# Performance work log

Measured on AMD Instinct MI355X. Metric: run time of the kernel, lower is better.

Reference implementation:

```python
import jax, jax.numpy as jnp
import numpy as np


def gcn_conv(x, W, b, src, dst, num_nodes):
    # PyG GCNConv: h = D^{-1/2} (A + I) D^{-1/2} (x W) + b
    h = x @ W  # [N, H]
    ones = jnp.ones(src.shape[0], dtype=h.dtype)
    deg = jax.ops.segment_sum(ones, dst, num_segments=num_nodes) + 1.0  # +1 for self-loop
    d_inv_sqrt = jax.lax.rsqrt(deg)
    norm = d_inv_sqrt[src] * d_inv_sqrt[dst]  # [E]
    msg = h[src] * norm[:, None]  # [E, H] gather
    agg = jax.ops.segment_sum(msg, dst, num_segments=num_nodes)  # scatter-add
    agg = agg + h * (1.0 / deg)[:, None]  # self-loop term: deg_i^{-1/2} * deg_i^{-1/2}
    return agg + b


def setup_inputs() -> dict:
    key = jax.random.key(0)
    ks = jax.random.split(key, 10)
    N, E, F, H, C, G = 100000, 1000000, 64, 128, 2, 512
    x = jax.random.normal(ks[0], (N, F), dtype=jnp.float32)
    edge_index = jax.random.randint(ks[1], (2, E), 0, N, dtype=jnp.int64)
    batch = jnp.sort(jax.random.randint(ks[2], (N,), 0, G, dtype=jnp.int64))
    s1 = 1.0 / np.sqrt(F)
    s2 = 1.0 / np.sqrt(H)
    W1 = jax.random.normal(ks[3], (F, H), dtype=jnp.float32) * s1
    b1 = jnp.zeros((H,), dtype=jnp.float32)
    W2 = jax.random.normal(ks[4], (H, H), dtype=jnp.float32) * s2
    b2 = jnp.zeros((H,), dtype=jnp.float32)
    Wfc = jax.random.normal(ks[5], (H, C), dtype=jnp.float32) * s2
    bfc = jnp.zeros((C,), dtype=jnp.float32)
    return {"x": x, "edge_index": edge_index, "batch": batch, "num_graphs": G,
            "W1": W1, "b1": b1, "W2": W2, "b2": b2, "Wfc": Wfc, "bfc": bfc}


def reference(x, edge_index, batch, num_graphs, W1, b1, W2, b2, Wfc, bfc):
    # Dropout is inference-mode (identity), matching model.eval().
    N = x.shape[0]
    src, dst = edge_index[0], edge_index[1]
    h = gcn_conv(x, W1, b1, src, dst, N)
    h = jax.nn.relu(h)
    h = gcn_conv(h, W2, b2, src, dst, N)
    h = jax.nn.relu(h)
    # global mean pool over graphs
    summed = jax.ops.segment_sum(h, batch, num_segments=num_graphs)  # [G, H]
    counts = jax.ops.segment_sum(jnp.ones((N,), h.dtype), batch, num_segments=num_graphs)
    pooled = summed / jnp.maximum(counts, 1.0)[:, None]
    logits = pooled @ Wfc + bfc  # [G, C]
    return jax.nn.softmax(logits, axis=1)
```

## Files before the change

### kernel.cpp

```cpp
#include <hip/hip_runtime.h>
#include <hip/hip_bf16.h>

typedef __hip_bfloat16 bf16;
typedef __attribute__((ext_vector_type(8))) short short8;
typedef __attribute__((ext_vector_type(4))) float f32x4;
typedef __attribute__((ext_vector_type(2))) float f32x2;

#define FDIM 64
#define HDIM 128

#define ESTRIDE 4096
#define EC 8192
#define ECPT (EC / 256)

__device__ __forceinline__ float b2f(bf16 v) { return __bfloat162float(v); }
__device__ __forceinline__ float bits2f(unsigned int u) {
    return __uint_as_float(u << 16);
}
__device__ __forceinline__ unsigned short f2bits(float f) {
    bf16 b = __float2bfloat16(f);
    return *reinterpret_cast<unsigned short*>(&b);
}
__device__ __forceinline__ unsigned char f2fp8(float v) {
    int pk = __builtin_amdgcn_cvt_pk_fp8_f32(v, v, 0, false);
    return (unsigned char)(pk & 0xFF);
}

__device__ __forceinline__ int edge_word(const int* e, long long logical_idx, int is64) {
    return is64 ? e[2 * logical_idx] : e[logical_idx];
}

__global__ __launch_bounds__(256) void k_phase1(const int* __restrict__ edge,
                                                int* __restrict__ gcur,
                                                int* __restrict__ ebuf,
                                                int E,
                                                const void* __restrict__ W1, const void* __restrict__ b1,
                                                const void* __restrict__ W2, const void* __restrict__ b2,
                                                const void* __restrict__ Wfc, const void* __restrict__ bfc,
                                                bf16* __restrict__ W1t, bf16* __restrict__ W2t,
                                                bf16* __restrict__ b1c, bf16* __restrict__ b2c,
                                                bf16* __restrict__ Wfcc, bf16* __restrict__ bfcc,
                                                const void* __restrict__ x,
                                                unsigned char* __restrict__ X8,
                                                int totalX4,
                                                int* __restrict__ flags,
                                                const int* __restrict__ batch,
                                                int* __restrict__ gstart,
                                                int N, int G,
                                                int NB1, int WB, int XB) {
    int blk = blockIdx.x;
    int tid = threadIdx.x;
    if (blk < NB1) {
        unsigned long long zb = __ballot(edge[2 * (tid & 63) + 1] == 0);
        int is64 = (__popcll(zb) > 32);
        __shared__ int h[512];
        for (int b2 = tid; b2 < 512; b2 += 256) h[b2] = 0;
        __syncthreads();
        int e0 = blk * EC;
        int dcache[ECPT];
#pragma unroll
        for (int k = 0; k < ECPT; k++) {
            int i = e0 + (k << 8) + tid;
            int d = -1;
            if (i < E) d = edge_word(edge, (long long)E + i, is64);
            dcache[k] = d;
            if (d >= 0) atomicAdd(&h[(d >> 8) & 511], 1);
        }
        __syncthreads();
        for (int b2 = tid; b2 < 512; b2 += 256) {
            int c = h[b2];
            h[b2] = c ? atomicAdd(&gcur[b2], c) : 0;
        }
        __syncthreads();
#pragma unroll
        for (int k = 0; k < ECPT; k++) {
            int i = e0 + (k << 8) + tid;
            int d = dcache[k];
            if (d >= 0) {
                int s = edge_word(edge, i, is64);
                int bb = (d >> 8) & 511;
                int pos = atomicAdd(&h[bb], 1);
                if ((unsigned)pos < (unsigned)ESTRIDE)
                    ebuf[(bb << 12) + pos] = s | ((d & 255) << 24);
            }
        }
    } else if (blk < NB1 + WB) {
        const unsigned short* w1u = (const unsigned short*)W1;
        unsigned short wv = w1u[2 * (tid & 63)];
        int ee = (wv >> 7) & 0xFF;
        unsigned long long wb2 = __ballot(ee == 0 || ee >= 137);
        int f0 = (__popcll(wb2) > 4);
        if (blk == NB1 && tid == 0) flags[0] = f0;
        int gid = (blk - NB1) * 256 + tid;
        int stride = WB * 256;
#define CV(src, si) (f0 ? __float2bfloat16(((const float*)(src))[si]) : ((const bf16*)(src))[si])
        for (int i = gid; i < FDIM * HDIM; i += stride) {
            int n = i >> 6, k = i & 63;
            W1t[i] = CV(W1, k * HDIM + n);
        }
        for (int i = gid; i < HDIM * HDIM; i += stride) {
            int n = i >> 7, k = i & 127;
            W2t[i] = CV(W2, k * HDIM + n);
        }
        for (int i = gid; i < HDIM; i += stride) b1c[i] = CV(b1, i);
        for (int i = gid; i < HDIM; i += stride) b2c[i] = CV(b2, i);
        for (int i = gid; i < HDIM * 2; i += stride) Wfcc[i] = CV(Wfc, i);
        for (int i = gid; i < 2; i += stride) bfcc[i] = CV(bfc, i);
#undef CV
    } else if (blk < NB1 + WB + XB) {
        const unsigned short* w1u = (const unsigned short*)W1;
        unsigned short wv = w1u[2 * (tid & 63)];
        int ee = (wv >> 7) & 0xFF;
        unsigned long long wb2 = __ballot(ee == 0 || ee >= 137);
        int f0 = (__popcll(wb2) > 4);
        int t = (blk - NB1 - WB) * 256 + tid;
        if (t >= totalX4) return;
        float4 v;
        if (f0) {
            v = ((const float4*)x)[t];
        } else {
            uint2 p = ((const uint2*)x)[t];
            v.x = bits2f(p.x & 0xFFFFu); v.y = bits2f(p.x >> 16);
            v.z = bits2f(p.y & 0xFFFFu); v.w = bits2f(p.y >> 16);
        }
        unsigned int q0 = (unsigned int)__builtin_amdgcn_cvt_pk_fp8_f32(v.x, v.y, 0, false) & 0xFFFFu;
        unsigned int q1 = (unsigned int)__builtin_amdgcn_cvt_pk_fp8_f32(v.z, v.w, 0, false) & 0xFFFFu;
        ((unsigned int*)X8)[t] = (q1 << 16) | q0;
    } else {
        int bv = batch[1025 + 2 * (tid & 63)];
        unsigned long long bb2 = __ballot(bv == 0);
        int is64 = (__popcll(bb2) > 32);
        int i = (blk - NB1 - WB - XB) * 256 + tid;
        if (i >= N) return;
        int bi = is64 ? batch[2 * i] : batch[i];
        if (i == 0) {
            for (int g = 0; g <= bi; g++) gstart[g] = 0;
        } else {
            int bp = is64 ? batch[2 * (i - 1)] : batch[i - 1];
            for (int g = bp + 1; g <= bi; g++) gstart[g] = i;
        }
        if (i == N - 1) {
            for (int g = bi + 1; g <= G; g++) gstart[g] = N;
        }
    }
}

__global__ __launch_bounds__(256) void k_csr(const int* __restrict__ ebuf,
                                             const int* __restrict__ gcur,
                                             int* __restrict__ rowptr,
                                             int* __restrict__ cnt,
                                             float* __restrict__ dinv,
                                             int* __restrict__ srclist,
                                             int* __restrict__ perm,
                                             int N) {
    __shared__ int sred[256];
    __shared__ int sc[256];
    __shared__ int sa[256], sb[256];
    __shared__ int dh[33];
    int b = blockIdx.x;
    int tid = threadIdx.x;
    int part = 0;
    for (int j = tid; j < b; j += 256) {
        int v = gcur[j];
        part += (v > ESTRIDE) ? ESTRIDE : v;
    }
    sred[tid] = part;
    __syncthreads();
    for (int s = 128; s > 0; s >>= 1) {
        if (tid < s) sred[tid] += sred[tid + s];
        __syncthreads();
    }
    int gbase = sred[0];
    int cnt_b = gcur[b];
    if (cnt_b > ESTRIDE) cnt_b = ESTRIDE;
    sc[tid] = 0;
    __syncthreads();
    const int* eb = ebuf + (b << 12);
    for (int j = tid; j < cnt_b; j += 256) {
        int p = eb[j];
        atomicAdd(&sc[(unsigned)p >> 24], 1);
    }
    __syncthreads();
    int cval = sc[tid];
    sa[tid] = cval;
    __syncthreads();
    int* cur = sa; int* nxt = sb;
    for (int off = 1; off < 256; off <<= 1) {
        int v = cur[tid];
        if (tid >= off) v += cur[tid - off];
        nxt[tid] = v;
        __syncthreads();
        int* t = cur; cur = nxt; nxt = t;
    }
    int excl = cur[tid] - cval;
    int node = (b << 8) + tid;
    if (node < N) {
        rowptr[node] = gbase + excl;
        cnt[node] = cval;
        dinv[node] = rsqrtf((float)cval + 1.0f);
    }
    __syncthreads();
    sc[tid] = excl;
    __syncthreads();
    for (int j = tid; j < cnt_b; j += 256) {
        int p = eb[j];
        int pos = atomicAdd(&sc[(unsigned)p >> 24], 1);
        srclist[gbase + pos] = p & 0xFFFFFF;
    }
    if (tid < 33) dh[tid] = 0;
    perm[(b << 8) + tid] = N;
    __syncthreads();
    int bin = -1;
    if (node < N) {
        int c = (cval < 32) ? cval : 32;
        bin = 32 - c;
        atomicAdd(&dh[bin], 1);
    }
    __syncthreads();
    if (tid == 0) {
        int acc2 = 0;
        for (int k = 0; k < 33; k++) { int t = dh[k]; dh[k] = acc2; acc2 += t; }
    }
    __syncthreads();
    if (bin >= 0) {
        int pos = atomicAdd(&dh[bin], 1);
        perm[(b << 8) + pos] = node;
    }
}

#define ACCFP8(u2, e) do { \
    f32x2 f01 = __builtin_amdgcn_cvt_pk_f32_fp8((u2).x, false); \
    f32x2 f23 = __builtin_amdgcn_cvt_pk_f32_fp8((u2).x, true); \
    f32x2 f45 = __builtin_amdgcn_cvt_pk_f32_fp8((u2).y, false); \
    f32x2 f67 = __builtin_amdgcn_cvt_pk_f32_fp8((u2).y, true); \
    acc[0] += f01[0] * (e); acc[1] += f01[1] * (e); \
    acc[2] += f23[0] * (e); acc[3] += f23[1] * (e); \
    acc[4] += f45[0] * (e); acc[5] += f45[1] * (e); \
    acc[6] += f67[0] * (e); acc[7] += f67[1] * (e); } while (0)

__global__ __launch_bounds__(256) void k_agg64(const unsigned char* __restrict__ x8,
                                               const int* __restrict__ srclist,
                                               const int* __restrict__ rowptr,
                                               const int* __restrict__ count,
                                               const float* __restrict__ dinv,
                                               const int* __restrict__ perm,
                                               bf16* __restrict__ outb, int N, int NR) {
    int wave = threadIdx.x >> 6;
    int lane = threadIdx.x & 63;
    int group = lane >> 3;
    int sub = lane & 7;
    int r = blockIdx.x * 32 + wave * 8 + group;
    int i = (r < NR) ? perm[r] : N;
    if (i >= N) return;
    int start = rowptr[i];
    int cnt = count[i];
    float di = dinv[i];
    const uint2* hrow = (const uint2*)x8;
    float acc[8] = {0.f, 0.f, 0.f, 0.f, 0.f, 0.f, 0.f, 0.f};
    int lb = group << 3;
    for (int jb = 0; jb < cnt; jb += 8) {
        int m = cnt - jb; if (m > 8) m = 8;
        int sv = srclist[start + jb + ((sub < m) ? sub : (m - 1))];
        float dvv = dinv[sv];
        if (m == 8) {
            int s[8]; float e[8]; uint2 v[8];
#pragma unroll
            for (int t = 0; t < 8; t++) { s[t] = __shfl(sv, lb + t); e[t] = __shfl(dvv, lb + t); }
#pragma unroll
            for (int t = 0; t < 8; t++) v[t] = hrow[(size_t)s[t] * 8 + sub];
#pragma unroll
            for (int t = 0; t < 8; t++) ACCFP8(v[t], e[t]);
        } else {
            int j = 0;
            for (; j + 4 <= m; j += 4) {
                int s0 = __shfl(sv, lb + j + 0); float e0 = __shfl(dvv, lb + j + 0);
                int s1 = __shfl(sv, lb + j + 1); float e1 = __shfl(dvv, lb + j + 1);
                int s2 = __shfl(sv, lb + j + 2); float e2 = __shfl(dvv, lb + j + 2);
                int s3 = __shfl(sv, lb + j + 3); float e3 = __shfl(dvv, lb + j + 3);
                uint2 v0 = hrow[(size_t)s0 * 8 + sub];
                uint2 v1 = hrow[(size_t)s1 * 8 + sub];
                uint2 v2 = hrow[(size_t)s2 * 8 + sub];
                uint2 v3 = hrow[(size_t)s3 * 8 + sub];
                ACCFP8(v0, e0); ACCFP8(v1, e1); ACCFP8(v2, e2); ACCFP8(v3, e3);
            }
            for (; j < m; j++) {
                int s0 = __shfl(sv, lb + j); float e0 = __shfl(dvv, lb + j);
                uint2 v0 = hrow[(size_t)s0 * 8 + sub];
                ACCFP8(v0, e0);
            }
        }
    }
    {
        uint2 vs = hrow[(size_t)i * 8 + sub];
        float self = di * di;
        float sacc[8] = {0.f};
        {
            float* acc = sacc;
            ACCFP8(vs, self);
        }
#pragma unroll
        for (int k = 0; k < 8; k++) acc[k] = di * acc[k] + sacc[k];
    }
    uint4 pv;
    pv.x = ((unsigned int)f2bits(acc[1]) << 16) | f2bits(acc[0]);
    pv.y = ((unsigned int)f2bits(acc[3]) << 16) | f2bits(acc[2]);
    pv.z = ((unsigned int)f2bits(acc[5]) << 16) | f2bits(acc[4]);
    pv.w = ((unsigned int)f2bits(acc[7]) << 16) | f2bits(acc[6]);
    ((uint4*)outb)[(size_t)i * 8 + sub] = pv;
}

__global__ __launch_bounds__(256) void k_agg128(const unsigned char* __restrict__ h8,
                                                const int* __restrict__ srclist,
                                                const int* __restrict__ rowptr,
                                                const int* __restrict__ count,
                                                const float* __restrict__ dinv,
                                                const int* __restrict__ perm,
                                                bf16* __restrict__ outb, int N, int NR) {
    int wave = threadIdx.x >> 6;
    int lane = threadIdx.x & 63;
    int group = lane >> 4;
    int sub = lane & 15;
    int r = blockIdx.x * 16 + wave * 4 + group;
    int i = (r < NR) ? perm[r] : N;
    if (i >= N) return;
    int start = rowptr[i];
    int cnt = count[i];
    float di = dinv[i];
    const uint2* hrow = (const uint2*)h8;
    float acc[8] = {0.f, 0.f, 0.f, 0.f, 0.f, 0.f, 0.f, 0.f};
    int lb = group << 4;
    for (int jb = 0; jb < cnt; jb += 16) {
        int m = cnt - jb; if (m > 16) m = 16;
        int sv = srclist[start + jb + ((sub < m) ? sub : (m - 1))];
        float dvv = dinv[sv];
        int j = 0;
        for (; j + 8 <= m; j += 8) {
            int s[8]; float e[8]; uint2 v[8];
#pragma unroll
            for (int t = 0; t < 8; t++) { s[t] = __shfl(sv, lb + j + t); e[t] = __shfl(dvv, lb + j + t); }
#pragma unroll
            for (int t = 0; t < 8; t++) v[t] = hrow[(size_t)s[t] * 16 + sub];
#pragma unroll
            for (int t = 0; t < 8; t++) ACCFP8(v[t], e[t]);
        }
        for (; j + 4 <= m; j += 4) {
            int s0 = __shfl(sv, lb + j + 0); float e0 = __shfl(dvv, lb + j + 0);
            int s1 = __shfl(sv, lb + j + 1); float e1 = __shfl(dvv, lb + j + 1);
            int s2 = __shfl(sv, lb + j + 2); float e2 = __shfl(dvv, lb + j + 2);
            int s3 = __shfl(sv, lb + j + 3); float e3 = __shfl(dvv, lb + j + 3);
            uint2 v0 = hrow[(size_t)s0 * 16 + sub];
            uint2 v1 = hrow[(size_t)s1 * 16 + sub];
            uint2 v2 = hrow[(size_t)s2 * 16 + sub];
            uint2 v3 = hrow[(size_t)s3 * 16 + sub];
            ACCFP8(v0, e0); ACCFP8(v1, e1); ACCFP8(v2, e2); ACCFP8(v3, e3);
        }
        for (; j < m; j++) {
            int s0 = __shfl(sv, lb + j); float e0 = __shfl(dvv, lb + j);
            uint2 v0 = hrow[(size_t)s0 * 16 + sub];
            ACCFP8(v0, e0);
        }
    }
    {
        uint2 vs = hrow[(size_t)i * 16 + sub];
        float self = di * di;
        float sacc[8] = {0.f};
        {
            float* acc = sacc;
            ACCFP8(vs, self);
        }
#pragma unroll
        for (int k = 0; k < 8; k++) acc[k] = di * acc[k] + sacc[k];
    }
    uint4 pv;
    pv.x = ((unsigned int)f2bits(acc[1]) << 16) | f2bits(acc[0]);
    pv.y = ((unsigned int)f2bits(acc[3]) << 16) | f2bits(acc[2]);
    pv.z = ((unsigned int)f2bits(acc[5]) << 16) | f2bits(acc[4]);
    pv.w = ((unsigned int)f2bits(acc[7]) << 16) | f2bits(acc[6]);
    ((uint4*)outb)[(size_t)i * 16 + sub] = pv;
}

#define K1PAD 72
__global__ __launch_bounds__(256) void k_gemmA(const bf16* __restrict__ Y,
                                               const bf16* __restrict__ W1t,
                                               const bf16* __restrict__ bias,
                                               unsigned char* __restrict__ h8, int N) {
    __shared__ bf16 As[64 * K1PAD];
    __shared__ bf16 Wt[HDIM * K1PAD];
    __shared__ float bsf[HDIM];
    int tid = threadIdx.x;
    int base = blockIdx.x * 64;
    {
        const uint4* wsrc = (const uint4*)W1t;
        for (int i = tid; i < HDIM * 8; i += 256) {
            int n = i >> 3, c = i & 7;
            *(uint4*)&Wt[n * K1PAD + c * 8] = wsrc[n * 8 + c];
        }
    }
    {
        const uint4* xb = (const uint4*)Y;
        for (int i = tid; i < 64 * 8; i += 256) {
            int r = i >> 3, c = i & 7;
            int gr = base + r; if (gr >= N) gr = N - 1;
            *(uint4*)&As[r * K1PAD + c * 8] = xb[(size_t)gr * 8 + c];
        }
    }
    if (tid < HDIM) bsf[tid] = b2f(bias[tid]);
    __syncthreads();
    int wid = tid >> 6, lane = tid & 63;
    int l15 = lane & 15, q = lane >> 4;
    int m0 = wid * 16;
    short8 af[2];
#pragma unroll
    for (int kc = 0; kc < 2; kc++)
        af[kc] = *(const short8*)&As[(m0 + l15) * K1PAD + kc * 32 + q * 8];
    f32x4 acc[8];
#pragma unroll
    for (int nt = 0; nt < 8; nt++) {
        acc[nt] = (f32x4){0.f, 0.f, 0.f, 0.f};
#pragma unroll
        for (int kc = 0; kc < 2; kc++) {
            short8 bf = *(const short8*)&Wt[(nt * 16 + l15) * K1PAD + kc * 32 + q * 8];
            acc[nt] = __builtin_amdgcn_mfma_f32_16x16x32_bf16(af[kc], bf, acc[nt], 0, 0, 0);
        }
    }
#pragma unroll
    for (int nt = 0; nt < 8; nt++) {
        int col = nt * 16 + l15;
        float bv = bsf[col];
#pragma unroll
        for (int r = 0; r < 4; r++) {
            int gr = base + m0 + q * 4 + r;
            if (gr < N) {
                float v = fmaxf(acc[nt][r] + bv, 0.f);
                h8[(size_t)gr * HDIM + col] = f2fp8(v);
            }
        }
    }
}

#define K2PAD 136
__global__ __launch_bounds__(256) void k_gemmB(const bf16* __restrict__ Z,
                                               const bf16* __restrict__ W2t,
                                               const bf16* __restrict__ bias,
                                               bf16* __restrict__ outp, int N) {
    __shared__ bf16 As[64 * K2PAD];
    __shared__ bf16 Wt[HDIM * K2PAD];
    __shared__ float bsf[HDIM];
    int tid = threadIdx.x;
    int base = blockIdx.x * 64;
    {
        const uint4* wsrc = (const uint4*)W2t;
        for (int i = tid; i < HDIM * 16; i += 256) {
            int n = i >> 4, c = i & 15;
            *(uint4*)&Wt[n * K2PAD + c * 8] = wsrc[n * 16 + c];
        }
    }
    const uint4* xb = (const uint4*)Z;
    for (int i = tid; i < 64 * 16; i += 256) {
        int r = i >> 4, c = i & 15;
        int gr = base + r; if (gr >= N) gr = N - 1;
        *(uint4*)&As[r * K2PAD + c * 8] = xb[(size_t)gr * 16 + c];
    }
    if (tid < HDIM) bsf[tid] = b2f(bias[tid]);
    __syncthreads();
    int wid = tid >> 6, lane = tid & 63;
    int l15 = lane & 15, q = lane >> 4;
    int m0 = wid * 16;
    short8 af[4];
#pragma unroll
    for (int kc = 0; kc < 4; kc++)
        af[kc] = *(const short8*)&As[(m0 + l15) * K2PAD + kc * 32 + q * 8];
    f32x4 acc[8];
#pragma unroll
    for (int nt = 0; nt < 8; nt++) {
        acc[nt] = (f32x4){0.f, 0.f, 0.f, 0.f};
#pragma unroll
        for (int kc = 0; kc < 4; kc++) {
            short8 bf = *(const short8*)&Wt[(nt * 16 + l15) * K2PAD + kc * 32 + q * 8];
            acc[nt] = __builtin_amdgcn_mfma_f32_16x16x32_bf16(af[kc], bf, acc[nt], 0, 0, 0);
        }
    }
#pragma unroll
    for (int nt = 0; nt < 8; nt++) {
        int col = nt * 16 + l15;
        float bv = bsf[col];
#pragma unroll
        for (int r = 0; r < 4; r++) {
            int gr = base + m0 + q * 4 + r;
            if (gr < N) outp[(size_t)gr * HDIM + col] = __float2bfloat16(fmaxf(acc[nt][r] + bv, 0.f));
        }
    }
}

__global__ __launch_bounds__(256) void k_pool(const bf16* __restrict__ hact,
                                              const int* __restrict__ gstart,
                                              const bf16* __restrict__ Wfc,
                                              const bf16* __restrict__ bfc,
                                              void* __restrict__ out,
                                              const int* __restrict__ flags) {
    __shared__ float lds[16][HDIM + 1];
    __shared__ float colsum[HDIM];
    int g = blockIdx.x;
    int s = gstart[g], e = gstart[g + 1];
    int tid = threadIdx.x;
    int cslot = tid & 15;
    int rslot = tid >> 4;
    const uint4* hp = (const uint4*)hact;
    float a[8] = {0.f, 0.f, 0.f, 0.f, 0.f, 0.f, 0.f, 0.f};
    for (int r = s + rslot; r < e; r += 16) {
        uint4 v = hp[(size_t)r * 16 + cslot];
        a[0] += bits2f(v.x & 0xFFFFu); a[1] += bits2f(v.x >> 16);
        a[2] += bits2f(v.y & 0xFFFFu); a[3] += bits2f(v.y >> 16);
        a[4] += bits2f(v.z & 0xFFFFu); a[5] += bits2f(v.z >> 16);
        a[6] += bits2f(v.w & 0xFFFFu); a[7] += bits2f(v.w >> 16);
    }
#pragma unroll
    for (int k = 0; k < 8; k++) lds[rslot][cslot * 8 + k] = a[k];
    __syncthreads();
    if (tid < HDIM) {
        float sum = 0.f;
#pragma unroll
        for (int k = 0; k < 16; k++) sum += lds[k][tid];
        colsum[tid] = sum;
    }
    __syncthreads();
    if (tid >= 64) return;
    int lane = tid;
    float inv = 1.0f / fmaxf((float)(e - s), 1.0f);
    float m0 = colsum[2 * lane] * inv;
    float m1 = colsum[2 * lane + 1] * inv;
    float l0 = m0 * b2f(Wfc[(2 * lane) * 2 + 0]) + m1 * b2f(Wfc[(2 * lane + 1) * 2 + 0]);
    float l1 = m0 * b2f(Wfc[(2 * lane) * 2 + 1]) + m1 * b2f(Wfc[(2 * lane + 1) * 2 + 1]);
    for (int sft = 32; sft; sft >>= 1) { l0 += __shfl_down(l0, sft); l1 += __shfl_down(l1, sft); }
    if (lane == 0) {
        float z0 = l0 + b2f(bfc[0]);
        float z1 = l1 + b2f(bfc[1]);
        float mx = fmaxf(z0, z1);
        float e0 = expf(z0 - mx), e1 = expf(z1 - mx);
        float sm = e0 + e1;
        float p0 = e0 / sm, p1 = e1 / sm;
        if (flags[0]) {
            ((float*)out)[2 * g + 0] = p0;
            ((float*)out)[2 * g + 1] = p1;
        } else {
            ((bf16*)out)[2 * g + 0] = __float2bfloat16(p0);
            ((bf16*)out)[2 * g + 1] = __float2bfloat16(p1);
        }
    }
}

extern "C" void kernel_launch(void* const* d_in, const int* in_sizes, int n_in,
                              void* d_out, int out_size, void* d_ws, size_t ws_size,
                              hipStream_t stream) {
    const void* x    = d_in[0];
    const int*  edge = (const int*)d_in[1];
    const int*  batch= (const int*)d_in[2];
    const void* W1  = d_in[4];
    const void* b1  = d_in[5];
    const void* W2  = d_in[6];
    const void* b2  = d_in[7];
    const void* Wfc = d_in[8];
    const void* bfc = d_in[9];

    int N = in_sizes[0] / FDIM;
    int E = in_sizes[1] / 2;
    int G = out_size / 2;

    int*   flags  = (int*)d_ws;
    float* dinv   = (float*)((char*)d_ws + 64);
    int*   gcur   = (int*)(dinv + N);
    int*   gstart = gcur + 512;
    int*   rowptr = gstart + 516;
    int*   count  = rowptr + N;
    int*   perm_  = count + N;
    int*   srclist= perm_ + 131072;
    int*   ebuf   = srclist + E;
    bf16*  Abuf   = (bf16*)(ebuf + 512 * ESTRIDE);
    bf16*  Bbuf   = Abuf + (size_t)N * HDIM;
    bf16*  b1c    = Bbuf + (size_t)N * HDIM;
    bf16*  b2c    = b1c + HDIM;
    bf16*  Wfcc   = b2c + HDIM;
    bf16*  bfcc   = Wfcc + 256;
    bf16*  W1t    = bfcc + 64;
    bf16*  W2t    = W1t + FDIM * HDIM;
    unsigned char* H8 = (unsigned char*)(W2t + HDIM * HDIM);
    unsigned char* X8 = H8 + (size_t)N * HDIM;

    bf16* Y = Abuf;
    bf16* Z = Abuf;

    int NB  = (N + 255) >> 8;
    int NR  = NB << 8;
    int NB1 = (E + EC - 1) / EC;
    int WB = 32;
    int XB = (N * 16 + 255) / 256;
    int BB = (N + 255) / 256;
    int totalX4 = N * 16;

    hipMemsetAsync(gcur, 0, 512 * sizeof(int), stream);
    k_phase1<<<NB1 + WB + XB + BB, 256, 0, stream>>>(edge, gcur, ebuf, E,
                                                     W1, b1, W2, b2, Wfc, bfc,
                                                     W1t, W2t, b1c, b2c, Wfcc, bfcc,
                                                     x, X8, totalX4, flags,
                                                     batch, gstart, N, G,
                                                     NB1, WB, XB);
    k_csr<<<NB, 256, 0, stream>>>(ebuf, gcur, rowptr, count, dinv, srclist, perm_, N);

    k_agg64<<<(NR + 31) / 32, 256, 0, stream>>>(X8, srclist, rowptr, count, dinv, perm_, Y, N, NR);
    k_gemmA<<<(N + 63) / 64, 256, 0, stream>>>(Y, W1t, b1c, H8, N);

    k_agg128<<<(NR + 15) / 16, 256, 0, stream>>>(H8, srclist, rowptr, count, dinv, perm_, Z, N, NR);
    k_gemmB<<<(N + 63) / 64, 256, 0, stream>>>(Z, W2t, b2c, Bbuf, N);

    k_pool<<<G, 256, 0, stream>>>(Bbuf, gstart, Wfcc, bfcc, d_out, flags);
}
```

Measured before the change: 245.6 us.

## Drop degree-sorted node permutation and widen aggregation lanes to 16-byte loads

Removes the per-block degree-binned permutation built in the CSR kernel, so both aggregation kernels process nodes in natural order. Each lane now loads 16 fp8 features (uint4) per neighbor instead of 8, halving lanes per node: 4 lanes per node for the 64-wide layer and 8 for the 128-wide layer. This cuts permutation overhead and the extra indirection, and widens memory transactions. In exchange, nodes with different degrees now share a wave, which can cause more divergence, and each lane holds more accumulator registers.

```diff
diff --git a/kernel.cpp b/kernel.cpp
--- a/kernel.cpp
+++ b/kernel.cpp
@@ -151,12 +151,10 @@
                                              int* __restrict__ cnt,
                                              float* __restrict__ dinv,
                                              int* __restrict__ srclist,
-                                             int* __restrict__ perm,
                                              int N) {
     __shared__ int sred[256];
     __shared__ int sc[256];
     __shared__ int sa[256], sb[256];
-    __shared__ int dh[33];
     int b = blockIdx.x;
     int tid = threadIdx.x;
     int part = 0;
@@ -207,69 +205,116 @@
         int pos = atomicAdd(&sc[(unsigned)p >> 24], 1);
         srclist[gbase + pos] = p & 0xFFFFFF;
     }
-    if (tid < 33) dh[tid] = 0;
-    perm[(b << 8) + tid] = N;
-    __syncthreads();
-    int bin = -1;
-    if (node < N) {
-        int c = (cval < 32) ? cval : 32;
-        bin = 32 - c;
-        atomicAdd(&dh[bin], 1);
-    }
-    __syncthreads();
-    if (tid == 0) {
-        int acc2 = 0;
-        for (int k = 0; k < 33; k++) { int t = dh[k]; dh[k] = acc2; acc2 += t; }
-    }
-    __syncthreads();
-    if (bin >= 0) {
-        int pos = atomicAdd(&dh[bin], 1);
-        perm[(b << 8) + pos] = node;
-    }
-}
-
-#define ACCFP8(u2, e) do { \
-    f32x2 f01 = __builtin_amdgcn_cvt_pk_f32_fp8((u2).x, false); \
-    f32x2 f23 = __builtin_amdgcn_cvt_pk_f32_fp8((u2).x, true); \
-    f32x2 f45 = __builtin_amdgcn_cvt_pk_f32_fp8((u2).y, false); \
-    f32x2 f67 = __builtin_amdgcn_cvt_pk_f32_fp8((u2).y, true); \
-    acc[0] += f01[0] * (e); acc[1] += f01[1] * (e); \
-    acc[2] += f23[0] * (e); acc[3] += f23[1] * (e); \
-    acc[4] += f45[0] * (e); acc[5] += f45[1] * (e); \
-    acc[6] += f67[0] * (e); acc[7] += f67[1] * (e); } while (0)
+}
+
+#define ACC4(w, e, o) do { \
+    f32x2 fA = __builtin_amdgcn_cvt_pk_f32_fp8((w), false); \
+    f32x2 fB = __builtin_amdgcn_cvt_pk_f32_fp8((w), true); \
+    acc[(o)+0] += fA[0] * (e); acc[(o)+1] += fA[1] * (e); \
+    acc[(o)+2] += fB[0] * (e); acc[(o)+3] += fB[1] * (e); } while (0)
+#define ACC16(u4, e) do { ACC4((u4).x, (e), 0); ACC4((u4).y, (e), 4); \
+                          ACC4((u4).z, (e), 8); ACC4((u4).w, (e), 12); } while (0)
+
+__device__ __forceinline__ uint4 packbf16x8(const float* a) {
+    uint4 p;
+    p.x = ((unsigned int)f2bits(a[1]) << 16) | f2bits(a[0]);
+    p.y = ((unsigned int)f2bits(a[3]) << 16) | f2bits(a[2]);
+    p.z = ((unsigned int)f2bits(a[5]) << 16) | f2bits(a[4]);
+    p.w = ((unsigned int)f2bits(a[7]) << 16) | f2bits(a[6]);
+    return p;
+}
 
 __global__ __launch_bounds__(256) void k_agg64(const unsigned char* __restrict__ x8,
                                                const int* __restrict__ srclist,
                                                const int* __restrict__ rowptr,
                                                const int* __restrict__ count,
                                                const float* __restrict__ dinv,
-                                               const int* __restrict__ perm,
-                                               bf16* __restrict__ outb, int N, int NR) {
+                                               bf16* __restrict__ outb, int N) {
+    int wave = threadIdx.x >> 6;
+    int lane = threadIdx.x & 63;
+    int group = lane >> 2;
+    int sub = lane & 3;
+    int i = blockIdx.x * 64 + wave * 16 + group;
+    if (i >= N) return;
+    int start = rowptr[i];
+    int cnt = count[i];
+    float di = dinv[i];
+    const uint4* hrow = (const uint4*)x8;
+    float acc[16];
+#pragma unroll
+    for (int k = 0; k < 16; k++) acc[k] = 0.f;
+    int lb = group << 2;
+    for (int jb = 0; jb < cnt; jb += 4) {
+        int m = cnt - jb; if (m > 4) m = 4;
+        int sv = srclist[start + jb + ((sub < m) ? sub : (m - 1))];
+        float dvv = dinv[sv];
+        if (m == 4) {
+            int s[4]; float e[4]; uint4 v[4];
+#pragma unroll
+            for (int t = 0; t < 4; t++) { s[t] = __shfl(sv, lb + t); e[t] = __shfl(dvv, lb + t); }
+#pragma unroll
+            for (int t = 0; t < 4; t++) v[t] = hrow[(size_t)s[t] * 4 + sub];
+#pragma unroll
+            for (int t = 0; t < 4; t++) ACC16(v[t], e[t]);
+        } else {
+            for (int j = 0; j < m; j++) {
+                int s0 = __shfl(sv, lb + j); float e0 = __shfl(dvv, lb + j);
+                uint4 v0 = hrow[(size_t)s0 * 4 + sub];
+                ACC16(v0, e0);
+            }
+        }
+    }
+    {
+        uint4 vs = hrow[(size_t)i * 4 + sub];
+        float self = di * di;
+        float sacc[16];
+#pragma unroll
+        for (int k = 0; k < 16; k++) sacc[k] = 0.f;
+        {
+            float* acc = sacc;
+            ACC16(vs, self);
+        }
+#pragma unroll
+        for (int k = 0; k < 16; k++) acc[k] = di * acc[k] + sacc[k];
+    }
+    uint4 p0 = packbf16x8(&acc[0]);
+    uint4 p1 = packbf16x8(&acc[8]);
+    ((uint4*)outb)[(size_t)i * 8 + sub * 2 + 0] = p0;
+    ((uint4*)outb)[(size_t)i * 8 + sub * 2 + 1] = p1;
+}
+
+__global__ __launch_bounds__(256) void k_agg128(const unsigned char* __restrict__ h8,
+                                                const int* __restrict__ srclist,
+                                                const int* __restrict__ rowptr,
+                                                const int* __restrict__ count,
+                                                const float* __restrict__ dinv,
+                                                bf16* __restrict__ outb, int N) {
     int wave = threadIdx.x >> 6;
     int lane = threadIdx.x & 63;
     int group = lane >> 3;
     int sub = lane & 7;
-    int r = blockIdx.x * 32 + wave * 8 + group;
-    int i = (r < NR) ? perm[r] : N;
+    int i = blockIdx.x * 32 + wave * 8 + group;
     if (i >= N) return;
     int start = rowptr[i];
     int cnt = count[i];
     float di = dinv[i];
-    const uint2* hrow = (const uint2*)x8;
-    float acc[8] = {0.f, 0.f, 0.f, 0.f, 0.f, 0.f, 0.f, 0.f};
+    const uint4* hrow = (const uint4*)h8;
+    float acc[16];
+#pragma unroll
+    for (int k = 0; k < 16; k++) acc[k] = 0.f;
     int lb = group << 3;
     for (int jb = 0; jb < cnt; jb += 8) {
         int m = cnt - jb; if (m > 8) m = 8;
         int sv = srclist[start + jb + ((sub < m) ? sub : (m - 1))];
         float dvv = dinv[sv];
         if (m == 8) {
-            int s[8]; float e[8]; uint2 v[8];
+            int s[8]; float e[8]; uint4 v[8];
 #pragma unroll
             for (int t = 0; t < 8; t++) { s[t] = __shfl(sv, lb + t); e[t] = __shfl(dvv, lb + t); }
 #pragma unroll
             for (int t = 0; t < 8; t++) v[t] = hrow[(size_t)s[t] * 8 + sub];
 #pragma unroll
-            for (int t = 0; t < 8; t++) ACCFP8(v[t], e[t]);
+            for (int t = 0; t < 8; t++) ACC16(v[t], e[t]);
         } else {
             int j = 0;
             for (; j + 4 <= m; j += 4) {
@@ -277,106 +322,36 @@
                 int s1 = __shfl(sv, lb + j + 1); float e1 = __shfl(dvv, lb + j + 1);
                 int s2 = __shfl(sv, lb + j + 2); float e2 = __shfl(dvv, lb + j + 2);
                 int s3 = __shfl(sv, lb + j + 3); float e3 = __shfl(dvv, lb + j + 3);
-                uint2 v0 = hrow[(size_t)s0 * 8 + sub];
-                uint2 v1 = hrow[(size_t)s1 * 8 + sub];
-                uint2 v2 = hrow[(size_t)s2 * 8 + sub];
-                uint2 v3 = hrow[(size_t)s3 * 8 + sub];
-                ACCFP8(v0, e0); ACCFP8(v1, e1); ACCFP8(v2, e2); ACCFP8(v3, e3);
+                uint4 v0 = hrow[(size_t)s0 * 8 + sub];
+                uint4 v1 = hrow[(size_t)s1 * 8 + sub];
+                uint4 v2 = hrow[(size_t)s2 * 8 + sub];
+                uint4 v3 = hrow[(size_t)s3 * 8 + sub];
+                ACC16(v0, e0); ACC16(v1, e1); ACC16(v2, e2); ACC16(v3, e3);
             }
             for (; j < m; j++) {
                 int s0 = __shfl(sv, lb + j); float e0 = __shfl(dvv, lb + j);
-                uint2 v0 = hrow[(size_t)s0 * 8 + sub];
-                ACCFP8(v0, e0);
+                uint4 v0 = hrow[(size_t)s0 * 8 + sub];
+                ACC16(v0, e0);
             }
         }
     }
     {
-        uint2 vs = hrow[(size_t)i * 8 + sub];
+        uint4 vs = hrow[(size_t)i * 8 + sub];
         float self = di * di;
-        float sacc[8] = {0.f};
+        float sacc[16];
+#pragma unroll
+        for (int k = 0; k < 16; k++) sacc[k] = 0.f;
         {
             float* acc = sacc;
-            ACCFP8(vs, self);
-        }
-#pragma unroll
-        for (int k = 0; k < 8; k++) acc[k] = di * acc[k] + sacc[k];
-    }
-    uint4 pv;
-    pv.x = ((unsigned int)f2bits(acc[1]) << 16) | f2bits(acc[0]);
-    pv.y = ((unsigned int)f2bits(acc[3]) << 16) | f2bits(acc[2]);
-    pv.z = ((unsigned int)f2bits(acc[5]) << 16) | f2bits(acc[4]);
-    pv.w = ((unsigned int)f2bits(acc[7]) << 16) | f2bits(acc[6]);
-    ((uint4*)outb)[(size_t)i * 8 + sub] = pv;
-}
-
-__global__ __launch_bounds__(256) void k_agg128(const unsigned char* __restrict__ h8,
-                                                const int* __restrict__ srclist,
-                                                const int* __restrict__ rowptr,
-                                                const int* __restrict__ count,
-                                                const float* __restrict__ dinv,
-                                                const int* __restrict__ perm,
-                                                bf16* __restrict__ outb, int N, int NR) {
-    int wave = threadIdx.x >> 6;
-    int lane = threadIdx.x & 63;
-    int group = lane >> 4;
-    int sub = lane & 15;
-    int r = blockIdx.x * 16 + wave * 4 + group;
-    int i = (r < NR) ? perm[r] : N;
-    if (i >= N) return;
-    int start = rowptr[i];
-    int cnt = count[i];
-    float di = dinv[i];
-    const uint2* hrow = (const uint2*)h8;
-    float acc[8] = {0.f, 0.f, 0.f, 0.f, 0.f, 0.f, 0.f, 0.f};
-    int lb = group << 4;
-    for (int jb = 0; jb < cnt; jb += 16) {
-        int m = cnt - jb; if (m > 16) m = 16;
-        int sv = srclist[start + jb + ((sub < m) ? sub : (m - 1))];
-        float dvv = dinv[sv];
-        int j = 0;
-        for (; j + 8 <= m; j += 8) {
-            int s[8]; float e[8]; uint2 v[8];
-#pragma unroll
-            for (int t = 0; t < 8; t++) { s[t] = __shfl(sv, lb + j + t); e[t] = __shfl(dvv, lb + j + t); }
-#pragma unroll
-            for (int t = 0; t < 8; t++) v[t] = hrow[(size_t)s[t] * 16 + sub];
-#pragma unroll
-            for (int t = 0; t < 8; t++) ACCFP8(v[t], e[t]);
-        }
-        for (; j + 4 <= m; j += 4) {
-            int s0 = __shfl(sv, lb + j + 0); float e0 = __shfl(dvv, lb + j + 0);
-            int s1 = __shfl(sv, lb + j + 1); float e1 = __shfl(dvv, lb + j + 1);
-            int s2 = __shfl(sv, lb + j + 2); float e2 = __shfl(dvv, lb + j + 2);
-            int s3 = __shfl(sv, lb + j + 3); float e3 = __shfl(dvv, lb + j + 3);
-            uint2 v0 = hrow[(size_t)s0 * 16 + sub];
-            uint2 v1 = hrow[(size_t)s1 * 16 + sub];
-            uint2 v2 = hrow[(size_t)s2 * 16 + sub];
-            uint2 v3 = hrow[(size_t)s3 * 16 + sub];
-            ACCFP8(v0, e0); ACCFP8(v1, e1); ACCFP8(v2, e2); ACCFP8(v3, e3);
-        }
-        for (; j < m; j++) {
-            int s0 = __shfl(sv, lb + j); float e0 = __shfl(dvv, lb + j);
-            uint2 v0 = hrow[(size_t)s0 * 16 + sub];
-            ACCFP8(v0, e0);
-        }
-    }
-    {
-        uint2 vs = hrow[(size_t)i * 16 + sub];
-        float self = di * di;
-        float sacc[8] = {0.f};
-        {
-            float* acc = sacc;
-            ACCFP8(vs, self);
-        }
-#pragma unroll
-        for (int k = 0; k < 8; k++) acc[k] = di * acc[k] + sacc[k];
-    }
-    uint4 pv;
-    pv.x = ((unsigned int)f2bits(acc[1]) << 16) | f2bits(acc[0]);
-    pv.y = ((unsigned int)f2bits(acc[3]) << 16) | f2bits(acc[2]);
-    pv.z = ((unsigned int)f2bits(acc[5]) << 16) | f2bits(acc[4]);
-    pv.w = ((unsigned int)f2bits(acc[7]) << 16) | f2bits(acc[6]);
-    ((uint4*)outb)[(size_t)i * 16 + sub] = pv;
+            ACC16(vs, self);
+        }
+#pragma unroll
+        for (int k = 0; k < 16; k++) acc[k] = di * acc[k] + sacc[k];
+    }
+    uint4 p0 = packbf16x8(&acc[0]);
+    uint4 p1 = packbf16x8(&acc[8]);
+    ((uint4*)outb)[(size_t)i * 16 + sub * 2 + 0] = p0;
+    ((uint4*)outb)[(size_t)i * 16 + sub * 2 + 1] = p1;
 }
 
 #define K1PAD 72
@@ -572,8 +547,7 @@
     int*   gstart = gcur + 512;
     int*   rowptr = gstart + 516;
     int*   count  = rowptr + N;
-    int*   perm_  = count + N;
-    int*   srclist= perm_ + 131072;
+    int*   srclist= count + N;
     int*   ebuf   = srclist + E;
     bf16*  Abuf   = (bf16*)(ebuf + 512 * ESTRIDE);
     bf16*  Bbuf   = Abuf + (size_t)N * HDIM;
@@ -590,7 +564,6 @@
     bf16* Z = Abuf;
 
     int NB  = (N + 255) >> 8;
-    int NR  = NB << 8;
     int NB1 = (E + EC - 1) / EC;
     int WB = 32;
     int XB = (N * 16 + 255) / 256;
@@ -604,12 +577,12 @@
                                                      x, X8, totalX4, flags,
                                                      batch, gstart, N, G,
                                                      NB1, WB, XB);
-    k_csr<<<NB, 256, 0, stream>>>(ebuf, gcur, rowptr, count, dinv, srclist, perm_, N);
-
-    k_agg64<<<(NR + 31) / 32, 256, 0, stream>>>(X8, srclist, rowptr, count, dinv, perm_, Y, N, NR);
+    k_csr<<<NB, 256, 0, stream>>>(ebuf, gcur, rowptr, count, dinv, srclist, N);
+
+    k_agg64<<<(N + 63) / 64, 256, 0, stream>>>(X8, srclist, rowptr, count, dinv, Y, N);
     k_gemmA<<<(N + 63) / 64, 256, 0, stream>>>(Y, W1t, b1c, H8, N);
 
-    k_agg128<<<(NR + 15) / 16, 256, 0, stream>>>(H8, srclist, rowptr, count, dinv, perm_, Z, N, NR);
+    k_agg128<<<(N + 31) / 32, 256, 0, stream>>>(H8, srclist, rowptr, count, dinv, Z, N);
     k_gemmB<<<(N + 63) / 64, 256, 0, stream>>>(Z, W2t, b2c, Bbuf, N);
 
     k_pool<<<G, 256, 0, stream>>>(Bbuf, gstart, Wfcc, bfcc, d_out, flags);
```

Measured after the change: 230.7 us. -6.1%, faster.
